# Kernel tuning notes

Measured on AMD Instinct MI355X. Metric: run time of the kernel, lower is better.

The kernel has to match this reference:

```python
import jax, jax.numpy as jnp
import numpy as np

N_NODES = 50000
N_EDGES = 800000
D = 128
N_LAYERS = 3
EPS = 1e-5  # torch LayerNorm default


def _gcn_conv(x, src, dst, dinv, W, b):
    # PyG GCNConv: h = x @ W; out[i] = sum_{(s->i)} dinv[s]*dinv[i]*h[s] + dinv[i]^2*h[i] + b
    h = x @ W
    norm = dinv[src] * dinv[dst]                      # [E]
    msgs = h[src] * norm[:, None]                     # [E, D] gather
    agg = jax.ops.segment_sum(msgs, dst, num_segments=N_NODES)  # scatter-add
    agg = agg + h * (dinv * dinv)[:, None]            # self-loop term
    return agg + b


def _layer_norm(x, gamma, beta):
    mu = jnp.mean(x, axis=-1, keepdims=True)
    var = jnp.mean(jnp.square(x - mu), axis=-1, keepdims=True)
    return (x - mu) * jax.lax.rsqrt(var + EPS) * gamma + beta


def setup_inputs() -> dict:
    key = jax.random.key(0)
    ks = jax.random.split(key, 4)
    x = jax.random.normal(ks[0], (N_NODES, D), dtype=jnp.float32)
    edge_index = jax.random.randint(ks[1], (2, N_EDGES), 0, N_NODES, dtype=jnp.int64)
    Ws = jax.random.normal(ks[2], (N_LAYERS, D, D), dtype=jnp.float32) * (1.0 / np.sqrt(D))
    bs = jnp.zeros((N_LAYERS, D), dtype=jnp.float32)
    gammas = jnp.ones((N_LAYERS, D), dtype=jnp.float32)
    betas = jnp.zeros((N_LAYERS, D), dtype=jnp.float32)
    return {"x": x, "edge_index": edge_index, "Ws": Ws, "bs": bs,
            "gammas": gammas, "betas": betas}


def reference(x, edge_index, Ws, bs, gammas, betas):
    src, dst = edge_index[0], edge_index[1]
    # GCN symmetric normalization with self-loops: deg[i] = in-degree(i) + 1
    deg = jnp.zeros((N_NODES,), dtype=x.dtype).at[dst].add(1.0) + 1.0
    dinv = jax.lax.rsqrt(deg)
    h = x
    for i in range(N_LAYERS):
        x_new = _gcn_conv(h, src, dst, dinv, Ws[i], bs[i])
        x_new = _layer_norm(x_new, gammas[i], betas[i])
        x_new = jax.nn.relu(x_new)  # dropout is identity in eval mode
        h = h + x_new if i > 0 else x_new
    return h
```

## Files before the change

### kernel.cpp

```cpp
#include <hip/hip_runtime.h>
#include <hip/hip_bf16.h>

#define NN 50000
#define NE 800000
#define DD 128
#define NB 196
#define NCH 8
#define CHSZ 6250
#define NC2 (NN * NCH)
#define NSB 391
#define PH (64 * NB)
#define FS 2048
#define NSL 391
#define HHB (NSL * 8)
#define CB 3125
#define WB 192
#define LN_EPS 1e-5f

typedef __bf16 bf16x8 __attribute__((ext_vector_type(8)));
typedef float f32x4 __attribute__((ext_vector_type(4)));

__device__ inline ushort f2bf_bits(float f) {
    union { __hip_bfloat16 h; ushort u; } c;
    c.h = __float2bfloat16(f);
    return c.u;
}

__global__ void hist_cast_kernel(const int* __restrict__ src, const int* __restrict__ dst,
                                 int* __restrict__ counts2, const float* __restrict__ x,
                                 uint4* __restrict__ fb0, const float* __restrict__ W,
                                 ushort* __restrict__ Wt) {
    int b = blockIdx.x;
    if (b < HHB) {
        int slice = b >> 3;
        int r = b & 7;
        int base = slice * FS;
#pragma unroll 2
        for (int i = threadIdx.x; i < FS; i += 256) {
            int e = base + i;
            if (e < NE) {
                int d = dst[e];
                if (d / CHSZ == r) {
                    int s = src[e];
                    atomicAdd(&counts2[d * NCH + s / CHSZ], 1);
                }
            }
        }
    } else if (b < HHB + CB) {
        int i = (b - HHB) * 256 + threadIdx.x;
        float4 v0 = ((const float4*)x)[2 * i];
        float4 v1 = ((const float4*)x)[2 * i + 1];
        union { ushort us[8]; uint4 u; } pk;
        pk.us[0] = f2bf_bits(v0.x); pk.us[1] = f2bf_bits(v0.y);
        pk.us[2] = f2bf_bits(v0.z); pk.us[3] = f2bf_bits(v0.w);
        pk.us[4] = f2bf_bits(v1.x); pk.us[5] = f2bf_bits(v1.y);
        pk.us[6] = f2bf_bits(v1.z); pk.us[7] = f2bf_bits(v1.w);
        fb0[i] = pk.u;
    } else {
        int i = (b - HHB - CB) * 256 + threadIdx.x;
        int l = i >> 14, k = (i >> 7) & 127, n = i & 127;
        Wt[l * 16384 + n * 128 + k] = f2bf_bits(W[i]);
    }
}

__global__ __launch_bounds__(1024) void scan1024_blocks(int* __restrict__ data,
                                                        int* __restrict__ bsums) {
    __shared__ int ws[16];
    int gid = blockIdx.x * 1024 + threadIdx.x;
    int lane = threadIdx.x & 63, wid = threadIdx.x >> 6;
    int v = (gid < NC2) ? data[gid] : 0;
    int x = v;
#pragma unroll
    for (int off = 1; off < 64; off <<= 1) {
        int t = __shfl_up(x, off, 64);
        if (lane >= off) x += t;
    }
    if (lane == 63) ws[wid] = x;
    __syncthreads();
    if (threadIdx.x == 0) {
        int run = 0;
        for (int i = 0; i < 16; ++i) { int t = ws[i]; ws[i] = run; run += t; }
        bsums[blockIdx.x] = run;
    }
    __syncthreads();
    if (gid < NC2) data[gid] = x - v + ws[wid];
}

__global__ __launch_bounds__(1024) void scan_sums1024(int* __restrict__ bsums, int nb) {
    __shared__ int ws[16];
    int tid = threadIdx.x;
    int lane = tid & 63, wid = tid >> 6;
    int v = (tid < nb) ? bsums[tid] : 0;
    int x = v;
#pragma unroll
    for (int off = 1; off < 64; off <<= 1) {
        int t = __shfl_up(x, off, 64);
        if (lane >= off) x += t;
    }
    if (lane == 63) ws[wid] = x;
    __syncthreads();
    if (tid == 0) {
        int run = 0;
        for (int i = 0; i < 16; ++i) { int t = ws[i]; ws[i] = run; run += t; }
    }
    __syncthreads();
    if (tid < nb) bsums[tid] = x - v + ws[wid];
}

__global__ void finalize_kernel(const int* __restrict__ excl2, const int* __restrict__ bsums,
                                int* __restrict__ row_ptr, int* __restrict__ next_pos2,
                                float* __restrict__ dinv, int* __restrict__ degarr,
                                int* __restrict__ bh) {
    __shared__ int lh[64];
    if (threadIdx.x < 64) lh[threadIdx.x] = 0;
    __syncthreads();
    int d = blockIdx.x * 256 + threadIdx.x;
    if (d < NN) {
        int base = d * NCH;
        int p0 = excl2[base] + bsums[base >> 10];
#pragma unroll
        for (int c = 0; c < NCH; ++c) {
            int idx = base + c;
            next_pos2[idx] = excl2[idx] + bsums[idx >> 10];
        }
        int nxt = (d == NN - 1) ? NE : excl2[base + NCH] + bsums[(base + NCH) >> 10];
        int deg = nxt - p0;
        row_ptr[d] = p0;
        dinv[d] = rsqrtf((float)deg + 1.0f);
        degarr[d] = deg;
        atomicAdd(&lh[min(deg, 63)], 1);
    }
    __syncthreads();
    if (threadIdx.x < 64) bh[threadIdx.x * NB + blockIdx.x] = lh[threadIdx.x];
    if (blockIdx.x == 0 && threadIdx.x == 0) row_ptr[NN] = NE;
}

__global__ __launch_bounds__(1024) void permscan_kernel(int* __restrict__ bh) {
    __shared__ int wsum[16];
    const int CH = 13;
    int tid = threadIdx.x;
    int base = tid * CH;
    int vals[CH];
    int s = 0;
#pragma unroll
    for (int i = 0; i < CH; ++i) {
        int idx = base + i;
        int v = (idx < PH) ? bh[idx] : 0;
        vals[i] = s;
        s += v;
    }
    int lane = tid & 63, wid = tid >> 6;
    int x = s;
#pragma unroll
    for (int off = 1; off < 64; off <<= 1) {
        int t = __shfl_up(x, off, 64);
        if (lane >= off) x += t;
    }
    if (lane == 63) wsum[wid] = x;
    __syncthreads();
    if (tid == 0) {
        int run = 0;
        for (int i = 0; i < 16; ++i) { int t = wsum[i]; wsum[i] = run; run += t; }
    }
    __syncthreads();
    int texcl = x - s + wsum[wid];
#pragma unroll
    for (int i = 0; i < CH; ++i) {
        int idx = base + i;
        if (idx < PH) bh[idx] = texcl + vals[i];
    }
}

__global__ void scatter_fill_kernel(const int* __restrict__ degarr, const int* __restrict__ bh,
                                    int* __restrict__ perm, const int* __restrict__ src,
                                    const int* __restrict__ dst, int* __restrict__ next_pos2,
                                    const float* __restrict__ dinv, int2* __restrict__ edge2) {
    if (blockIdx.x < NB) {
        __shared__ int lh[64];
        __shared__ int lbase[64];
        if (threadIdx.x < 64) {
            lh[threadIdx.x] = 0;
            lbase[threadIdx.x] = bh[threadIdx.x * NB + blockIdx.x];
        }
        __syncthreads();
        int gid = blockIdx.x * 256 + threadIdx.x;
        if (gid < NN) {
            int b = min(degarr[gid], 63);
            int r = atomicAdd(&lh[b], 1);
            perm[lbase[b] + r] = gid;
        }
    } else {
        int bb = blockIdx.x - NB;
        int slice = bb >> 3;
        int r = bb & 7;
        int base = slice * FS;
#pragma unroll 2
        for (int i = threadIdx.x; i < FS; i += 256) {
            int e = base + i;
            if (e < NE) {
                int d = dst[e];
                if (d / CHSZ == r) {
                    int s = src[e];
                    int pos = atomicAdd(&next_pos2[d * NCH + s / CHSZ], 1);
                    int2 o;
                    o.x = s;
                    o.y = __float_as_int(dinv[s] * dinv[d]);
                    edge2[pos] = o;
                }
            }
        }
    }
}

template <bool RES, bool FINAL>
__global__ __launch_bounds__(256) void layer_kernel(
    const ushort* __restrict__ fin, const int* __restrict__ row_ptr,
    const int2* __restrict__ edge2, const int* __restrict__ perm,
    const float* __restrict__ dinv, const ushort* __restrict__ Wt,
    const float* __restrict__ bias, const float* __restrict__ gamma,
    const float* __restrict__ beta, ushort* __restrict__ fout, float* __restrict__ out) {
    __shared__ uint4 sA[16 * 17];
    __shared__ int sNode[16];
    __shared__ float sLN1[4][16], sLN2[4][16];

    int w = threadIdx.x >> 6, lane = threadIdx.x & 63;
    int g = lane >> 4, t = lane & 15;
    int arow = w * 4 + g;
    int slot = blockIdx.x * 16 + arow;
    int node = perm[slot];
    if (t == 0) sNode[arow] = node;

    {
        int beg = row_ptr[node], end = row_ptr[node + 1];
        const uint4* cu4 = (const uint4*)fin;
        float acc[8] = {};
        int e = beg;
        for (; e + 4 <= end; e += 4) {
            int2 a[4];
            uint4 v[4];
#pragma unroll
            for (int j = 0; j < 4; ++j) a[j] = edge2[e + j];
#pragma unroll
            for (int j = 0; j < 4; ++j) v[j] = cu4[a[j].x * 16 + t];
#pragma unroll
            for (int j = 0; j < 4; ++j) {
                uint vv[4] = {v[j].x, v[j].y, v[j].z, v[j].w};
                float ww = __int_as_float(a[j].y);
#pragma unroll
                for (int i = 0; i < 4; ++i) {
                    acc[2 * i] = fmaf(ww, __uint_as_float(vv[i] << 16), acc[2 * i]);
                    acc[2 * i + 1] =
                        fmaf(ww, __uint_as_float(vv[i] & 0xffff0000u), acc[2 * i + 1]);
                }
            }
        }
        for (; e < end; ++e) {
            int2 a = edge2[e];
            uint4 v = cu4[a.x * 16 + t];
            uint vv[4] = {v.x, v.y, v.z, v.w};
            float ww = __int_as_float(a.y);
#pragma unroll
            for (int i = 0; i < 4; ++i) {
                acc[2 * i] = fmaf(ww, __uint_as_float(vv[i] << 16), acc[2 * i]);
                acc[2 * i + 1] = fmaf(ww, __uint_as_float(vv[i] & 0xffff0000u), acc[2 * i + 1]);
            }
        }
        float di = dinv[node];
        float w2s = di * di;
        {
            uint4 v = cu4[node * 16 + t];
            uint vv[4] = {v.x, v.y, v.z, v.w};
#pragma unroll
            for (int i = 0; i < 4; ++i) {
                acc[2 * i] = fmaf(w2s, __uint_as_float(vv[i] << 16), acc[2 * i]);
                acc[2 * i + 1] = fmaf(w2s, __uint_as_float(vv[i] & 0xffff0000u), acc[2 * i + 1]);
            }
        }
        union { ushort us[8]; uint4 u; } pk;
#pragma unroll
        for (int i = 0; i < 8; ++i) pk.us[i] = f2bf_bits(acc[i]);
        sA[arow * 17 + t] = pk.u;
    }
    __syncthreads();

    int q = lane >> 4, m = lane & 15;
    f32x4 c0 = (f32x4){0.f, 0.f, 0.f, 0.f};
    f32x4 c1 = (f32x4){0.f, 0.f, 0.f, 0.f};
    int n0 = 16 * (2 * w), n1 = 16 * (2 * w + 1);
#pragma unroll
    for (int kk = 0; kk < 4; ++kk) {
        bf16x8 af = *(const bf16x8*)&sA[m * 17 + kk * 4 + q];
        bf16x8 b0 = *(const bf16x8*)(Wt + (n0 + m) * DD + kk * 32 + q * 8);
        bf16x8 b1 = *(const bf16x8*)(Wt + (n1 + m) * DD + kk * 32 + q * 8);
        c0 = __builtin_amdgcn_mfma_f32_16x16x32_bf16(af, b0, c0, 0, 0, 0);
        c1 = __builtin_amdgcn_mfma_f32_16x16x32_bf16(af, b1, c1, 0, 0, 0);
    }

    float bb0 = bias[n0 + m], bb1 = bias[n1 + m];
    float s1[4], s2[4];
#pragma unroll
    for (int r = 0; r < 4; ++r) {
        float v0 = c0[r] + bb0, v1 = c1[r] + bb1;
        c0[r] = v0; c1[r] = v1;
        s1[r] = v0 + v1;
        s2[r] = v0 * v0 + v1 * v1;
    }
#pragma unroll
    for (int off = 1; off <= 8; off <<= 1) {
#pragma unroll
        for (int r = 0; r < 4; ++r) {
            s1[r] += __shfl_xor(s1[r], off, 64);
            s2[r] += __shfl_xor(s2[r], off, 64);
        }
    }
    if (m == 0) {
#pragma unroll
        for (int r = 0; r < 4; ++r) {
            sLN1[w][q * 4 + r] = s1[r];
            sLN2[w][q * 4 + r] = s2[r];
        }
    }
    __syncthreads();
    float ga0 = gamma[n0 + m], ga1 = gamma[n1 + m];
    float be0 = beta[n0 + m], be1 = beta[n1 + m];
#pragma unroll
    for (int r = 0; r < 4; ++r) {
        int row = q * 4 + r;
        float S1 = sLN1[0][row] + sLN1[1][row] + sLN1[2][row] + sLN1[3][row];
        float S2 = sLN2[0][row] + sLN2[1][row] + sLN2[2][row] + sLN2[3][row];
        float mu = S1 * (1.f / 128.f);
        float var = S2 * (1.f / 128.f) - mu * mu;
        float rstd = rsqrtf(var + LN_EPS);
        int nd = sNode[row];
        size_t rb = (size_t)nd * DD;
        float o0 = fmaxf((c0[r] - mu) * rstd * ga0 + be0, 0.f);
        float o1 = fmaxf((c1[r] - mu) * rstd * ga1 + be1, 0.f);
        if (RES) {
            o0 += __uint_as_float(((uint)fin[rb + n0 + m]) << 16);
            o1 += __uint_as_float(((uint)fin[rb + n1 + m]) << 16);
        }
        if (FINAL) {
            out[rb + n0 + m] = o0;
            out[rb + n1 + m] = o1;
        } else {
            fout[rb + n0 + m] = f2bf_bits(o0);
            fout[rb + n1 + m] = f2bf_bits(o1);
        }
    }
}


extern "C" void kernel_launch(void* const* d_in, const int* in_sizes, int n_in,
                              void* d_out, int out_size, void* d_ws, size_t ws_size,
                              hipStream_t stream) {
    const float* x = (const float*)d_in[0];
    const int* edge = (const int*)d_in[1];
    const float* Ws = (const float*)d_in[2];
    const float* bs = (const float*)d_in[3];
    const float* gs = (const float*)d_in[4];
    const float* bes = (const float*)d_in[5];
    float* out = (float*)d_out;
    const int* src = edge;
    const int* dst = edge + NE;

    char* p = (char*)d_ws;
    int* counts2 = (int*)p;     p += (size_t)NC2 * 4;
    int* bsums = (int*)p;       p += 1024 * 4;
    int* row_ptr = (int*)p;     p += (size_t)(NN + 4) * 4;
    int* next_pos2 = (int*)p;   p += (size_t)NC2 * 4;
    float* dinv = (float*)p;    p += (size_t)NN * 4;
    int* degarr = (int*)p;      p += (size_t)NN * 4;
    int* bh = (int*)p;          p += (size_t)PH * 4;
    int* perm = (int*)p;        p += (size_t)NN * 4;
    int2* edge2 = (int2*)p;     p += (size_t)NE * 8;
    ushort* fb0 = (ushort*)p;   p += (size_t)NN * DD * 2;
    ushort* fb1 = (ushort*)p;   p += (size_t)NN * DD * 2;
    ushort* Wt = (ushort*)p;    p += (size_t)3 * DD * DD * 2;

    hipMemsetAsync(counts2, 0, (size_t)NC2 * 4, stream);
    hist_cast_kernel<<<HHB + CB + WB, 256, 0, stream>>>(src, dst, counts2, x, (uint4*)fb0, Ws,
                                                        Wt);
    scan1024_blocks<<<NSB, 1024, 0, stream>>>(counts2, bsums);
    scan_sums1024<<<1, 1024, 0, stream>>>(bsums, NSB);
    finalize_kernel<<<NB, 256, 0, stream>>>(counts2, bsums, row_ptr, next_pos2, dinv, degarr,
                                            bh);
    permscan_kernel<<<1, 1024, 0, stream>>>(bh);
    scatter_fill_kernel<<<NB + NSL * 8, 256, 0, stream>>>(degarr, bh, perm, src, dst,
                                                          next_pos2, dinv, edge2);

    int lg = NN / 16;
    layer_kernel<false, false><<<lg, 256, 0, stream>>>(
        fb0, row_ptr, edge2, perm, dinv, Wt, bs, gs, bes, fb1, out);
    layer_kernel<true, false><<<lg, 256, 0, stream>>>(
        fb1, row_ptr, edge2, perm, dinv, Wt + 16384, bs + DD, gs + DD, bes + DD, fb0, out);
    layer_kernel<true, true><<<lg, 256, 0, stream>>>(
        fb0, row_ptr, edge2, perm, dinv, Wt + 32768, bs + 2 * DD, gs + 2 * DD, bes + 2 * DD,
        fb1, out);
}
```

Before: 312.1 us.

## Quantize gathered node features to int8 with per-row scales

The input cast and each layer's epilogue now also produce an int8 copy of the node features with one float scale per row. The edge aggregation gathers from this int8 copy, folding the row scale into the edge weight. This halves the bytes fetched per gathered neighbour row compared with bf16. The cost is an extra int8 write and a row-max reduction with an added barrier per layer, plus accuracy loss from 8-bit quantization that may not meet the tolerance.

New measurement: 301.2 us. 1.04x faster.

```diff
diff --git a/kernel.cpp b/kernel.cpp
--- a/kernel.cpp
+++ b/kernel.cpp
@@ -13,7 +13,7 @@
 #define FS 2048
 #define NSL 391
 #define HHB (NSL * 8)
-#define CB 3125
+#define QB 3125
 #define WB 192
 #define LN_EPS 1e-5f
 
@@ -28,8 +28,8 @@
 
 __global__ void hist_cast_kernel(const int* __restrict__ src, const int* __restrict__ dst,
                                  int* __restrict__ counts2, const float* __restrict__ x,
-                                 uint4* __restrict__ fb0, const float* __restrict__ W,
-                                 ushort* __restrict__ Wt) {
+                                 uint2* __restrict__ qf0, float* __restrict__ sc0,
+                                 const float* __restrict__ W, ushort* __restrict__ Wt) {
     int b = blockIdx.x;
     if (b < HHB) {
         int slice = b >> 3;
@@ -46,18 +46,35 @@
                 }
             }
         }
-    } else if (b < HHB + CB) {
-        int i = (b - HHB) * 256 + threadIdx.x;
-        float4 v0 = ((const float4*)x)[2 * i];
-        float4 v1 = ((const float4*)x)[2 * i + 1];
-        union { ushort us[8]; uint4 u; } pk;
-        pk.us[0] = f2bf_bits(v0.x); pk.us[1] = f2bf_bits(v0.y);
-        pk.us[2] = f2bf_bits(v0.z); pk.us[3] = f2bf_bits(v0.w);
-        pk.us[4] = f2bf_bits(v1.x); pk.us[5] = f2bf_bits(v1.y);
-        pk.us[6] = f2bf_bits(v1.z); pk.us[7] = f2bf_bits(v1.w);
-        fb0[i] = pk.u;
+    } else if (b < HHB + QB) {
+        int bb = b - HHB;
+        int group = threadIdx.x >> 4, t = threadIdx.x & 15;
+        int node = bb * 16 + group;
+        const float4* xr = (const float4*)(x + (size_t)node * DD + t * 8);
+        float4 v0 = xr[0], v1 = xr[1];
+        float vals[8] = {v0.x, v0.y, v0.z, v0.w, v1.x, v1.y, v1.z, v1.w};
+        float am = 0.f;
+#pragma unroll
+        for (int i = 0; i < 8; ++i) am = fmaxf(am, fabsf(vals[i]));
+#pragma unroll
+        for (int off = 1; off <= 8; off <<= 1) am = fmaxf(am, __shfl_xor(am, off, 64));
+        float inv = 127.f / fmaxf(am, 1e-20f);
+        uint lo = 0, hi = 0;
+#pragma unroll
+        for (int i = 0; i < 4; ++i) {
+            int q = __float2int_rn(vals[i] * inv);
+            lo |= ((uint)(q & 0xff)) << (8 * i);
+        }
+#pragma unroll
+        for (int i = 0; i < 4; ++i) {
+            int q = __float2int_rn(vals[4 + i] * inv);
+            hi |= ((uint)(q & 0xff)) << (8 * i);
+        }
+        uint2 pk; pk.x = lo; pk.y = hi;
+        qf0[node * 16 + t] = pk;
+        if (t == 0) sc0[node] = am / 127.f;
     } else {
-        int i = (b - HHB - CB) * 256 + threadIdx.x;
+        int i = (b - HHB - QB) * 256 + threadIdx.x;
         int l = i >> 14, k = (i >> 7) & 127, n = i & 127;
         Wt[l * 16384 + n * 128 + k] = f2bf_bits(W[i]);
     }
@@ -214,14 +231,17 @@
 
 template <bool RES, bool FINAL>
 __global__ __launch_bounds__(256) void layer_kernel(
+    const uint2* __restrict__ qin, const float* __restrict__ scin,
     const ushort* __restrict__ fin, const int* __restrict__ row_ptr,
     const int2* __restrict__ edge2, const int* __restrict__ perm,
     const float* __restrict__ dinv, const ushort* __restrict__ Wt,
     const float* __restrict__ bias, const float* __restrict__ gamma,
-    const float* __restrict__ beta, ushort* __restrict__ fout, float* __restrict__ out) {
+    const float* __restrict__ beta, ushort* __restrict__ fout, char* __restrict__ qfout,
+    float* __restrict__ scout, float* __restrict__ out) {
     __shared__ uint4 sA[16 * 17];
     __shared__ int sNode[16];
     __shared__ float sLN1[4][16], sLN2[4][16];
+    __shared__ float sMX[4][16];
 
     int w = threadIdx.x >> 6, lane = threadIdx.x & 63;
     int g = lane >> 4, t = lane & 15;
@@ -232,49 +252,60 @@
 
     {
         int beg = row_ptr[node], end = row_ptr[node + 1];
-        const uint4* cu4 = (const uint4*)fin;
         float acc[8] = {};
         int e = beg;
         for (; e + 4 <= end; e += 4) {
             int2 a[4];
-            uint4 v[4];
+            uint2 qv[4];
+            float sc[4];
 #pragma unroll
             for (int j = 0; j < 4; ++j) a[j] = edge2[e + j];
 #pragma unroll
-            for (int j = 0; j < 4; ++j) v[j] = cu4[a[j].x * 16 + t];
-#pragma unroll
             for (int j = 0; j < 4; ++j) {
-                uint vv[4] = {v[j].x, v[j].y, v[j].z, v[j].w};
-                float ww = __int_as_float(a[j].y);
-#pragma unroll
-                for (int i = 0; i < 4; ++i) {
-                    acc[2 * i] = fmaf(ww, __uint_as_float(vv[i] << 16), acc[2 * i]);
-                    acc[2 * i + 1] =
-                        fmaf(ww, __uint_as_float(vv[i] & 0xffff0000u), acc[2 * i + 1]);
-                }
+                qv[j] = qin[a[j].x * 16 + t];
+                sc[j] = scin[a[j].x];
+            }
+#pragma unroll
+            for (int j = 0; j < 4; ++j) {
+                float ww = __int_as_float(a[j].y) * sc[j];
+                uint lo = qv[j].x, hi = qv[j].y;
+                acc[0] = fmaf(ww, (float)(char)(lo), acc[0]);
+                acc[1] = fmaf(ww, (float)(char)(lo >> 8), acc[1]);
+                acc[2] = fmaf(ww, (float)(char)(lo >> 16), acc[2]);
+                acc[3] = fmaf(ww, (float)(char)(lo >> 24), acc[3]);
+                acc[4] = fmaf(ww, (float)(char)(hi), acc[4]);
+                acc[5] = fmaf(ww, (float)(char)(hi >> 8), acc[5]);
+                acc[6] = fmaf(ww, (float)(char)(hi >> 16), acc[6]);
+                acc[7] = fmaf(ww, (float)(char)(hi >> 24), acc[7]);
             }
         }
         for (; e < end; ++e) {
             int2 a = edge2[e];
-            uint4 v = cu4[a.x * 16 + t];
-            uint vv[4] = {v.x, v.y, v.z, v.w};
-            float ww = __int_as_float(a.y);
-#pragma unroll
-            for (int i = 0; i < 4; ++i) {
-                acc[2 * i] = fmaf(ww, __uint_as_float(vv[i] << 16), acc[2 * i]);
-                acc[2 * i + 1] = fmaf(ww, __uint_as_float(vv[i] & 0xffff0000u), acc[2 * i + 1]);
-            }
-        }
-        float di = dinv[node];
-        float w2s = di * di;
+            uint2 qv = qin[a.x * 16 + t];
+            float ww = __int_as_float(a.y) * scin[a.x];
+            uint lo = qv.x, hi = qv.y;
+            acc[0] = fmaf(ww, (float)(char)(lo), acc[0]);
+            acc[1] = fmaf(ww, (float)(char)(lo >> 8), acc[1]);
+            acc[2] = fmaf(ww, (float)(char)(lo >> 16), acc[2]);
+            acc[3] = fmaf(ww, (float)(char)(lo >> 24), acc[3]);
+            acc[4] = fmaf(ww, (float)(char)(hi), acc[4]);
+            acc[5] = fmaf(ww, (float)(char)(hi >> 8), acc[5]);
+            acc[6] = fmaf(ww, (float)(char)(hi >> 16), acc[6]);
+            acc[7] = fmaf(ww, (float)(char)(hi >> 24), acc[7]);
+        }
         {
-            uint4 v = cu4[node * 16 + t];
-            uint vv[4] = {v.x, v.y, v.z, v.w};
-#pragma unroll
-            for (int i = 0; i < 4; ++i) {
-                acc[2 * i] = fmaf(w2s, __uint_as_float(vv[i] << 16), acc[2 * i]);
-                acc[2 * i + 1] = fmaf(w2s, __uint_as_float(vv[i] & 0xffff0000u), acc[2 * i + 1]);
-            }
+            float di = dinv[node];
+            uint2 qv = qin[node * 16 + t];
+            float ww = di * di * scin[node];
+            uint lo = qv.x, hi = qv.y;
+            acc[0] = fmaf(ww, (float)(char)(lo), acc[0]);
+            acc[1] = fmaf(ww, (float)(char)(lo >> 8), acc[1]);
+            acc[2] = fmaf(ww, (float)(char)(lo >> 16), acc[2]);
+            acc[3] = fmaf(ww, (float)(char)(lo >> 24), acc[3]);
+            acc[4] = fmaf(ww, (float)(char)(hi), acc[4]);
+            acc[5] = fmaf(ww, (float)(char)(hi >> 8), acc[5]);
+            acc[6] = fmaf(ww, (float)(char)(hi >> 16), acc[6]);
+            acc[7] = fmaf(ww, (float)(char)(hi >> 24), acc[7]);
         }
         union { ushort us[8]; uint4 u; } pk;
 #pragma unroll
@@ -323,6 +354,7 @@
     __syncthreads();
     float ga0 = gamma[n0 + m], ga1 = gamma[n1 + m];
     float be0 = beta[n0 + m], be1 = beta[n1 + m];
+    float o0v[4], o1v[4], rmax[4];
 #pragma unroll
     for (int r = 0; r < 4; ++r) {
         int row = q * 4 + r;
@@ -345,6 +377,32 @@
         } else {
             fout[rb + n0 + m] = f2bf_bits(o0);
             fout[rb + n1 + m] = f2bf_bits(o1);
+            o0v[r] = o0; o1v[r] = o1;
+            rmax[r] = fmaxf(o0, o1);
+        }
+    }
+    if (!FINAL) {
+#pragma unroll
+        for (int off = 1; off <= 8; off <<= 1) {
+#pragma unroll
+            for (int r = 0; r < 4; ++r) rmax[r] = fmaxf(rmax[r], __shfl_xor(rmax[r], off, 64));
+        }
+        if (m == 0) {
+#pragma unroll
+            for (int r = 0; r < 4; ++r) sMX[w][q * 4 + r] = rmax[r];
+        }
+        __syncthreads();
+#pragma unroll
+        for (int r = 0; r < 4; ++r) {
+            int row = q * 4 + r;
+            float M = fmaxf(fmaxf(sMX[0][row], sMX[1][row]), fmaxf(sMX[2][row], sMX[3][row]));
+            float inv = 127.f / fmaxf(M, 1e-20f);
+            int nd = sNode[row];
+            if (w == 0 && m == 0) scout[nd] = M / 127.f;
+            int q0 = min(__float2int_rn(o0v[r] * inv), 127);
+            int q1 = min(__float2int_rn(o1v[r] * inv), 127);
+            qfout[(size_t)nd * DD + n0 + m] = (char)q0;
+            qfout[(size_t)nd * DD + n1 + m] = (char)q1;
         }
     }
 }
@@ -375,11 +433,15 @@
     int2* edge2 = (int2*)p;     p += (size_t)NE * 8;
     ushort* fb0 = (ushort*)p;   p += (size_t)NN * DD * 2;
     ushort* fb1 = (ushort*)p;   p += (size_t)NN * DD * 2;
+    char* qf0 = (char*)p;       p += (size_t)NN * DD;
+    char* qf1 = (char*)p;       p += (size_t)NN * DD;
+    float* sc0 = (float*)p;     p += (size_t)NN * 4;
+    float* sc1 = (float*)p;     p += (size_t)NN * 4;
     ushort* Wt = (ushort*)p;    p += (size_t)3 * DD * DD * 2;
 
     hipMemsetAsync(counts2, 0, (size_t)NC2 * 4, stream);
-    hist_cast_kernel<<<HHB + CB + WB, 256, 0, stream>>>(src, dst, counts2, x, (uint4*)fb0, Ws,
-                                                        Wt);
+    hist_cast_kernel<<<HHB + QB + WB, 256, 0, stream>>>(src, dst, counts2, x, (uint2*)qf0,
+                                                        sc0, Ws, Wt);
     scan1024_blocks<<<NSB, 1024, 0, stream>>>(counts2, bsums);
     scan_sums1024<<<1, 1024, 0, stream>>>(bsums, NSB);
     finalize_kernel<<<NB, 256, 0, stream>>>(counts2, bsums, row_ptr, next_pos2, dinv, degarr,
@@ -390,10 +452,12 @@
 
     int lg = NN / 16;
     layer_kernel<false, false><<<lg, 256, 0, stream>>>(
-        fb0, row_ptr, edge2, perm, dinv, Wt, bs, gs, bes, fb1, out);
+        (const uint2*)qf0, sc0, fb0, row_ptr, edge2, perm, dinv, Wt, bs, gs, bes,
+        fb1, qf1, sc1, out);
     layer_kernel<true, false><<<lg, 256, 0, stream>>>(
-        fb1, row_ptr, edge2, perm, dinv, Wt + 16384, bs + DD, gs + DD, bes + DD, fb0, out);
+        (const uint2*)qf1, sc1, fb1, row_ptr, edge2, perm, dinv, Wt + 16384, bs + DD, gs + DD,
+        bes + DD, fb0, qf0, sc0, out);
     layer_kernel<true, true><<<lg, 256, 0, stream>>>(
-        fb0, row_ptr, edge2, perm, dinv, Wt + 32768, bs + 2 * DD, gs + 2 * DD, bes + 2 * DD,
-        fb1, out);
-}
+        (const uint2*)qf0, sc0, fb0, row_ptr, edge2, perm, dinv, Wt + 32768, bs + 2 * DD,
+        gs + 2 * DD, bes + 2 * DD, fb1, qf1, sc1, out);
+}
```
